# Performance work log

Measured on AMD Instinct MI355X. Metric: run time of the kernel, lower is better.

## Reference

```python
import jax, jax.numpy as jnp
import numpy as np
import math

D_MODEL = 1024
NUM_HEADS = 16
MAX_LEN = 2048
D_HEAD = D_MODEL // NUM_HEADS
BATCH = 2
SEQ = 2048


def setup_inputs() -> dict:
    root = jax.random.key(0)
    ks = jax.random.split(root, 10)
    s = 1.0 / math.sqrt(D_MODEL)
    return {
        "query": jax.random.normal(ks[0], (BATCH, SEQ, D_MODEL), jnp.float32),
        "key": jax.random.normal(ks[1], (BATCH, SEQ, D_MODEL), jnp.float32),
        "value": jax.random.normal(ks[2], (BATCH, SEQ, D_MODEL), jnp.float32),
        "Wq": jax.random.normal(ks[3], (D_MODEL, D_MODEL), jnp.float32) * s,
        "bq": jax.random.normal(ks[4], (D_MODEL,), jnp.float32) * s,
        "Wk": jax.random.normal(ks[5], (D_MODEL, D_MODEL), jnp.float32) * s,
        "bk": jax.random.normal(ks[6], (D_MODEL,), jnp.float32) * s,
        "Wv": jax.random.normal(ks[7], (D_MODEL, D_MODEL), jnp.float32) * s,
        "bv": jax.random.normal(ks[8], (D_MODEL,), jnp.float32) * s,
        "Er": jax.random.normal(ks[9], (MAX_LEN, D_HEAD), jnp.float32),
    }


def _skew(QEr):
    # QEr: [B, H, S, S] -> pad one zero column on the left, reshape, drop first row
    B, H, R, C = QEr.shape
    padded = jnp.pad(QEr, ((0, 0), (0, 0), (0, 0), (1, 0)))  # [B,H,R,C+1]
    reshaped = padded.reshape(B, H, C + 1, R)
    return reshaped[:, :, 1:, :]  # [B,H,R,C] == Srel


def reference(query, key, value, Wq, bq, Wk, bk, Wv, bv, Er):
    B, S, D = query.shape
    H, dh = NUM_HEADS, D_HEAD
    # nn.Linear: x @ W.T + b
    q = (jnp.einsum("bsd,ed->bse", query, Wq) + bq).reshape(B, S, H, dh).transpose(0, 2, 1, 3)  # [B,H,S,dh]
    k = (jnp.einsum("bsd,ed->bse", key, Wk) + bk).reshape(B, S, H, dh).transpose(0, 2, 1, 3)
    v = (jnp.einsum("bsd,ed->bse", value, Wv) + bv).reshape(B, S, H, dh).transpose(0, 2, 1, 3)
    start = MAX_LEN - S
    Er_s = Er[start:, :]  # [S, dh]
    QEr = jnp.einsum("bhsd,ld->bhsl", q, Er_s)  # [B,H,S,S]
    Srel = _skew(QEr)
    QK = jnp.einsum("bhsd,bhtd->bhst", q, k)
    attn = (QK + Srel) / math.sqrt(dh)
    causal = jnp.tril(jnp.ones((S, S), dtype=bool))
    attn = jnp.where(causal[None, None], attn, -jnp.inf)
    attn = jax.nn.softmax(attn, axis=-1)
    out = jnp.einsum("bhst,bhtd->bhsd", attn, v)  # [B,H,S,dh]
    out = out.transpose(0, 2, 1, 3).reshape(B, S, D)
    return out  # dropout is identity in eval mode
```

## Files before the change

kernel.cpp:

```cpp
#include <hip/hip_runtime.h>
#include <hip/hip_bf16.h>

typedef __attribute__((ext_vector_type(8))) short bf16x8;
typedef __attribute__((ext_vector_type(4))) float f32x4;

#define DEVI __device__ __forceinline__

constexpr int SEQ_   = 2048;
constexpr int HEADS  = 16;
constexpr int DHEAD  = 64;
constexpr int DMODEL = 1024;

DEVI unsigned short f2bf(float x) {
  __hip_bfloat16 h = __float2bfloat16(x);
  return __builtin_bit_cast(unsigned short, h);
}

DEVI f32x4 MFMA(bf16x8 a, bf16x8 b, f32x4 c) {
  return __builtin_amdgcn_mfma_f32_16x16x32_bf16(a, b, c, 0, 0, 0);
}

__global__ void conv3_kernel(const float* s0, const float* s1, const float* s2,
                             unsigned short* d0, unsigned short* d1, unsigned short* d2,
                             int n) {
  const float* s = (blockIdx.y == 0) ? s0 : (blockIdx.y == 1) ? s1 : s2;
  unsigned short* d = (blockIdx.y == 0) ? d0 : (blockIdx.y == 1) ? d1 : d2;
  int i = (blockIdx.x * 256 + threadIdx.x) * 8;
  if (i >= n) return;
  const float4* p = (const float4*)(s + i);
  float4 v0 = p[0], v1 = p[1];
  union { unsigned short u[8]; bf16x8 v; } t;
  t.u[0] = f2bf(v0.x); t.u[1] = f2bf(v0.y); t.u[2] = f2bf(v0.z); t.u[3] = f2bf(v0.w);
  t.u[4] = f2bf(v1.x); t.u[5] = f2bf(v1.y); t.u[6] = f2bf(v1.z); t.u[7] = f2bf(v1.w);
  *(bf16x8*)(d + i) = t.v;
}

__global__ __launch_bounds__(256) void proj3_kernel(
    const unsigned short* __restrict__ X0, const unsigned short* __restrict__ X1,
    const unsigned short* __restrict__ X2,
    const unsigned short* __restrict__ W0, const unsigned short* __restrict__ W1,
    const unsigned short* __restrict__ W2,
    const float* __restrict__ bi0, const float* __restrict__ bi1,
    const float* __restrict__ bi2,
    unsigned short* __restrict__ o0, unsigned short* __restrict__ o1,
    unsigned short* __restrict__ o2) {
  const int z = blockIdx.z;
  const unsigned short* X = (z == 0) ? X0 : (z == 1) ? X1 : X2;
  const unsigned short* W = (z == 0) ? W0 : (z == 1) ? W1 : W2;
  const float* bias        = (z == 0) ? bi0 : (z == 1) ? bi1 : bi2;
  unsigned short* out      = (z == 0) ? o0 : (z == 1) ? o1 : o2;

  __shared__ unsigned short Abuf[2][128 * 32];
  __shared__ unsigned short Bbuf[2][128 * 32];
  const int tid  = threadIdx.x;
  const int lane = tid & 63, wv = tid >> 6;
  const int q = lane >> 4, r = lane & 15;
  const int wrow = wv >> 1, wcol = wv & 1;
  const int rowA0 = blockIdx.x * 128, colB0 = blockIdx.y * 128;

  const char* Ag = (const char*)(X + (size_t)rowA0 * DMODEL);
  const char* Bg = (const char*)(W + (size_t)colB0 * DMODEL);

  f32x4 acc[4][4] = {};

  auto stage = [&](int ks, int buf) {
    const int koff = ks * 64;
#pragma unroll
    for (int i = 0; i < 2; ++i) {
      const int b   = (i * 256 + tid) * 16;
      const int row = b >> 6, col = b & 63;
      __builtin_amdgcn_global_load_lds(
          (const __attribute__((address_space(1))) void*)(Ag + (size_t)row * (DMODEL * 2) + koff + col),
          (__attribute__((address_space(3))) void*)((char*)&Abuf[buf][0] + i * 4096 + wv * 1024),
          16, 0, 0);
      __builtin_amdgcn_global_load_lds(
          (const __attribute__((address_space(1))) void*)(Bg + (size_t)row * (DMODEL * 2) + koff + col),
          (__attribute__((address_space(3))) void*)((char*)&Bbuf[buf][0] + i * 4096 + wv * 1024),
          16, 0, 0);
    }
  };

  stage(0, 0);
  for (int ks = 0; ks < 32; ++ks) {
    __syncthreads();
    if (ks + 1 < 32) stage(ks + 1, (ks + 1) & 1);
    const unsigned short* A  = &Abuf[ks & 1][0];
    const unsigned short* Bt = &Bbuf[ks & 1][0];
    bf16x8 af[4], bfr[4];
#pragma unroll
    for (int t = 0; t < 4; ++t) {
      af[t]  = *(const bf16x8*)(A  + (wrow * 64 + t * 16 + r) * 32 + q * 8);
      bfr[t] = *(const bf16x8*)(Bt + (wcol * 64 + t * 16 + r) * 32 + q * 8);
    }
#pragma unroll
    for (int m = 0; m < 4; ++m)
#pragma unroll
      for (int n = 0; n < 4; ++n)
        acc[m][n] = MFMA(af[m], bfr[n], acc[m][n]);
  }

#pragma unroll
  for (int m = 0; m < 4; ++m) {
#pragma unroll
    for (int n = 0; n < 4; ++n) {
      const int e  = colB0 + wcol * 64 + n * 16 + r;
      const float bv = bias[e];
      const int h = e >> 6, dd = e & 63;
      const int nrow0 = rowA0 + wrow * 64 + m * 16 + q * 4;
      const int bb = nrow0 >> 11, ss0 = nrow0 & 2047;
      const size_t bh = (size_t)(bb * HEADS + h);
      if (z == 0) {
#pragma unroll
        for (int j = 0; j < 4; ++j)
          out[(bh * SEQ_ + (ss0 + j)) * DHEAD + dd] = f2bf(acc[m][n][j] + bv);
      } else if (z == 1) {
#pragma unroll
        for (int j = 0; j < 4; ++j) {
          const int s = ss0 + j;
          const size_t off = (bh * 64 + (size_t)(s >> 5)) * 2048
                           + (size_t)(((dd >> 5) * 2 + ((s >> 4) & 1)) * 512)
                           + (size_t)(((((dd & 31) >> 3) << 4) + (s & 15)) * 8)
                           + (dd & 7);
          out[off] = f2bf(acc[m][n][j] + bv);
        }
      } else {
        union { unsigned short u[4]; uint2 v; } pk;
#pragma unroll
        for (int j = 0; j < 4; ++j) pk.u[j] = f2bf(acc[m][n][j] + bv);
        const size_t off = (bh * 64 + (size_t)(ss0 >> 5)) * 2048
                         + (size_t)((dd >> 4) * 512)
                         + (size_t)(((((ss0 & 31) >> 3) << 4) + (dd & 15)) * 8)
                         + (ss0 & 7);
        *(uint2*)&out[off] = pk.v;
      }
    }
  }
}

__global__ __launch_bounds__(128, 4) void attn_kernel(const unsigned short* __restrict__ qb,
                                                      const unsigned short* __restrict__ kt,
                                                      const unsigned short* __restrict__ vt,
                                                      const unsigned short* __restrict__ Er,
                                                      float* __restrict__ out,
                                                      float* __restrict__ pO,
                                                      float* __restrict__ pL) {
  __shared__ unsigned short k_lds[2][2048];
  __shared__ unsigned short v_lds[2][2048];
  __shared__ unsigned short p_lds[2][16][40];

  const int tid  = threadIdx.x;
  const int lane = tid & 63, wv = tid >> 6;
  const int q = lane >> 4, r = lane & 15;

  const int lid = blockIdx.x;
  const int xcd = lid & 7, idx = lid >> 3;
  const int bh  = (xcd << 2) | (idx & 3);
  const int rest = idx >> 2;
  const int p = rest >> 1, ab = rest & 1;
  const int Lt = 63 - p;
  const int sid = (bh << 5) | p;
  const int bb = bh >> 4, hh = bh & 15;

  const unsigned short* qbh = qb + (size_t)bh * SEQ_ * DHEAD;
  const char* ktb = (const char*)(kt + (size_t)bh * 64 * 2048);
  const char* vtb = (const char*)(vt + (size_t)bh * 64 * 2048);

  const f32x4 zero4 = {0.f, 0.f, 0.f, 0.f};

  auto stage = [&](int ktile, int buf) {
#pragma unroll
    for (int c = 0; c < 2; ++c) {
      __builtin_amdgcn_global_load_lds(
          (const __attribute__((address_space(1))) void*)(ktb + (size_t)ktile * 4096 + (c * 128 + tid) * 16),
          (__attribute__((address_space(3))) void*)((char*)&k_lds[buf][0] + c * 2048 + wv * 1024),
          16, 0, 0);
      __builtin_amdgcn_global_load_lds(
          (const __attribute__((address_space(1))) void*)(vtb + (size_t)ktile * 4096 + (c * 128 + tid) * 16),
          (__attribute__((address_space(3))) void*)((char*)&v_lds[buf][0] + c * 2048 + wv * 1024),
          16, 0, 0);
    }
  };

  auto run_strip = [&](int tile, int it0, int itN, float* po, float* pl) {
    const int s0 = tile * 32 + wv * 16;
    __syncthreads();
    stage(it0, 0);

    bf16x8 qf0 = *(const bf16x8*)(qbh + (size_t)(s0 + r) * DHEAD + q * 8);
    bf16x8 qf1 = *(const bf16x8*)(qbh + (size_t)(s0 + r) * DHEAD + 32 + q * 8);

    f32x4 oacc[4] = {};
    float lpart[4] = {0.f, 0.f, 0.f, 0.f};
    f32x4 qer0;
    {
      const int l0 = 2032 + it0 * 32 - s0 + r;
      bf16x8 e00 = *(const bf16x8*)(Er + (size_t)l0 * DHEAD + q * 8);
      bf16x8 e01 = *(const bf16x8*)(Er + (size_t)l0 * DHEAD + 32 + q * 8);
      qer0 = MFMA(qf1, e01, MFMA(qf0, e00, zero4));
    }

#pragma unroll 1
    for (int it = it0; it < itN; ++it) {
      const int cur = (it - it0) & 1;
      const int t0 = it * 32;
      const int lbase = 2032 + t0 - s0;

      __syncthreads();

      int l1 = lbase + 16 + r; l1 = l1 < 2047 ? l1 : 2047;
      int l2 = lbase + 32 + r; l2 = l2 < 2047 ? l2 : 2047;
      bf16x8 e10 = *(const bf16x8*)(Er + (size_t)l1 * DHEAD + q * 8);
      bf16x8 e11 = *(const bf16x8*)(Er + (size_t)l1 * DHEAD + 32 + q * 8);
      bf16x8 e20 = *(const bf16x8*)(Er + (size_t)l2 * DHEAD + q * 8);
      bf16x8 e21 = *(const bf16x8*)(Er + (size_t)l2 * DHEAD + 32 + q * 8);

      if (it + 1 < itN) stage(it + 1, 1 - cur);

      const unsigned short* KL = &k_lds[cur][0];
      const unsigned short* VL = &v_lds[cur][0];
      bf16x8 kf00 = *(const bf16x8*)(KL + lane * 8);
      bf16x8 kf10 = *(const bf16x8*)(KL + 512 + lane * 8);
      bf16x8 kf01 = *(const bf16x8*)(KL + 1024 + lane * 8);
      bf16x8 kf11 = *(const bf16x8*)(KL + 1536 + lane * 8);

      __builtin_amdgcn_s_setprio(1);
      f32x4 s40  = MFMA(qf1, kf01, MFMA(qf0, kf00, zero4));
      f32x4 s41  = MFMA(qf1, kf11, MFMA(qf0, kf10, zero4));
      f32x4 qer1 = MFMA(qf1, e11, MFMA(qf0, e10, zero4));
      f32x4 qer2 = MFMA(qf1, e21, MFMA(qf0, e20, zero4));
      __builtin_amdgcn_s_setprio(0);

#pragma unroll
      for (int j = 0; j < 4; ++j) {
        const int sl = q * 4 + j;
        const int idxw = r + 15 - sl;
        const int srcl = (q << 4) | (idxw & 15);
        const float g0 = __shfl(qer0[j], srcl);
        const float g1 = __shfl(qer1[j], srcl);
        const float g2 = __shfl(qer2[j], srcl);
        const bool lo = (idxw < 16);
        float sv0 = (s40[j] + (lo ? g0 : g1)) * 0.125f;
        float sv1 = (s41[j] + (lo ? g1 : g2)) * 0.125f;
        if (t0 + r      > s0 + sl) sv0 = -1e30f;
        if (t0 + 16 + r > s0 + sl) sv1 = -1e30f;
        const float p0 = __expf(sv0);
        const float p1 = __expf(sv1);
        lpart[j] += p0 + p1;
        p_lds[wv][sl][r]      = f2bf(p0);
        p_lds[wv][sl][16 + r] = f2bf(p1);
      }

      bf16x8 pf  = *(const bf16x8*)(&p_lds[wv][r][0] + q * 8);
      bf16x8 vf0 = *(const bf16x8*)(VL + lane * 8);
      bf16x8 vf1 = *(const bf16x8*)(VL + 512 + lane * 8);
      bf16x8 vf2 = *(const bf16x8*)(VL + 1024 + lane * 8);
      bf16x8 vf3 = *(const bf16x8*)(VL + 1536 + lane * 8);
      __builtin_amdgcn_s_setprio(1);
      oacc[0] = MFMA(pf, vf0, oacc[0]);
      oacc[1] = MFMA(pf, vf1, oacc[1]);
      oacc[2] = MFMA(pf, vf2, oacc[2]);
      oacc[3] = MFMA(pf, vf3, oacc[3]);
      __builtin_amdgcn_s_setprio(0);
      qer0 = qer2;
    }

#pragma unroll
    for (int j = 0; j < 4; ++j) {
      float ls = lpart[j];
#pragma unroll
      for (int d = 1; d < 16; d <<= 1) ls += __shfl_xor(ls, d);
      const int row = wv * 16 + q * 4 + j;
      if (po) {
#pragma unroll
        for (int dc = 0; dc < 4; ++dc)
          po[(size_t)row * 64 + dc * 16 + r] = oacc[dc][j];
        if (r == 0) pl[row] = ls;
      } else {
        const float inv = 1.0f / ls;
        const int ss = tile * 32 + row;
#pragma unroll
        for (int dc = 0; dc < 4; ++dc) {
          const int dd = dc * 16 + r;
          out[((size_t)(bb * SEQ_ + ss)) * DMODEL + hh * DHEAD + dd] = oacc[dc][j] * inv;
        }
      }
    }
  };

  if (ab == 0) {
    run_strip(Lt, 0, 32, pO + (size_t)(sid * 2) * 2048, pL + (size_t)(sid * 2) * 32);
  } else {
    run_strip(Lt, 32, 64 - p, pO + (size_t)(sid * 2 + 1) * 2048, pL + (size_t)(sid * 2 + 1) * 32);
    run_strip(p, 0, p + 1, nullptr, nullptr);
  }
}

__global__ __launch_bounds__(256) void reduce_kernel(const float* __restrict__ pO,
                                                     const float* __restrict__ pL,
                                                     float* __restrict__ out) {
  const int sid = blockIdx.x;
  const int bh = sid >> 5, p = sid & 31;
  const int bb = bh >> 4, hh = bh & 15;
  const int srow = (63 - p) * 32;
  const int tid = threadIdx.x;
  const int row = tid >> 3, dseg = (tid & 7) * 8;

  const float* a = pO + (size_t)(sid * 2) * 2048 + row * 64 + dseg;
  const float* b = a + 2048;
  const float la = pL[(size_t)(sid * 2) * 32 + row];
  const float lb = pL[(size_t)(sid * 2 + 1) * 32 + row];
  const float inv = 1.0f / (la + lb);

  float4 x0 = ((const float4*)a)[0], x1 = ((const float4*)a)[1];
  float4 y0 = ((const float4*)b)[0], y1 = ((const float4*)b)[1];
  float4 o0, o1;
  o0.x = (x0.x + y0.x) * inv; o0.y = (x0.y + y0.y) * inv;
  o0.z = (x0.z + y0.z) * inv; o0.w = (x0.w + y0.w) * inv;
  o1.x = (x1.x + y1.x) * inv; o1.y = (x1.y + y1.y) * inv;
  o1.z = (x1.z + y1.z) * inv; o1.w = (x1.w + y1.w) * inv;

  float* dst = out + ((size_t)(bb * SEQ_) + srow + row) * DMODEL + hh * DHEAD + dseg;
  ((float4*)dst)[0] = o0;
  ((float4*)dst)[1] = o1;
}

extern "C" void kernel_launch(void* const* d_in, const int* in_sizes, int n_in,
                              void* d_out, int out_size, void* d_ws, size_t ws_size,
                              hipStream_t stream) {
  const float* query = (const float*)d_in[0];
  const float* key   = (const float*)d_in[1];
  const float* value = (const float*)d_in[2];
  const float* Wq    = (const float*)d_in[3];
  const float* bq    = (const float*)d_in[4];
  const float* Wk    = (const float*)d_in[5];
  const float* bk    = (const float*)d_in[6];
  const float* Wv    = (const float*)d_in[7];
  const float* bv    = (const float*)d_in[8];
  const float* Er    = (const float*)d_in[9];

  char* ws = (char*)d_ws;
  unsigned short* qb   = (unsigned short*)(ws + (0u  << 20));
  unsigned short* ktil = (unsigned short*)(ws + (8u  << 20));
  unsigned short* vtil = (unsigned short*)(ws + (16u << 20));
  float*          pO   = (float*)(ws + (24u << 20));
  float*          pL   = (float*)(ws + (40u << 20));
  unsigned short* Xq   = (unsigned short*)(ws + (32u << 20));
  unsigned short* Xk   = (unsigned short*)(ws + (40u << 20));
  unsigned short* Xv   = (unsigned short*)(ws + (48u << 20));
  unsigned short* Wqb  = (unsigned short*)(ws + (56u << 20));
  unsigned short* Wkb  = (unsigned short*)(ws + (58u << 20));
  unsigned short* Wvb  = (unsigned short*)(ws + (60u << 20));
  unsigned short* Erb  = (unsigned short*)(ws + (62u << 20));

  conv3_kernel<<<dim3(2048, 3), 256, 0, stream>>>(query, key, value, Xq, Xk, Xv,
                                                  2 * SEQ_ * DMODEL);
  conv3_kernel<<<dim3(512, 3), 256, 0, stream>>>(Wq, Wk, Wv, Wqb, Wkb, Wvb,
                                                 DMODEL * DMODEL);
  conv3_kernel<<<dim3(64, 1), 256, 0, stream>>>(Er, Er, Er, Erb, Erb, Erb,
                                                SEQ_ * DHEAD);

  proj3_kernel<<<dim3(32, 8, 3), 256, 0, stream>>>(Xq, Xk, Xv, Wqb, Wkb, Wvb,
                                                   bq, bk, bv, qb, ktil, vtil);

  attn_kernel<<<dim3(2048), 128, 0, stream>>>(qb, ktil, vtil, Erb,
                                              (float*)d_out, pO, pL);

  reduce_kernel<<<dim3(1024), 256, 0, stream>>>(pO, pL, (float*)d_out);
}
```

Before: 155.3 us.

## Restructure relative attention into 128-row tiles with interleaved key-tile split

The attention kernel now runs 256-thread blocks, where each wave handles 32 query rows, so every staged K/V tile is shared across twice as many rows. Key tiles are split by parity between two blocks per query tile, and each block processes one long and one short tile to balance causal work. The reduce kernel is rewritten to combine those partials over 128-row tiles, and the 1/sqrt(dh) scale is folded into the Q projection epilogue. In exchange, each iteration does more Er loads and Er-projection MFMAs per row tile, since the old carried qer reuse is gone. The kernel also launches fewer blocks and needs more registers per thread.

New measurement: 155.9 us. Within noise of the previous version (+0.4%).

```diff
diff --git a/kernel.cpp b/kernel.cpp
--- a/kernel.cpp
+++ b/kernel.cpp
@@ -112,7 +112,7 @@
       if (z == 0) {
 #pragma unroll
         for (int j = 0; j < 4; ++j)
-          out[(bh * SEQ_ + (ss0 + j)) * DHEAD + dd] = f2bf(acc[m][n][j] + bv);
+          out[(bh * SEQ_ + (ss0 + j)) * DHEAD + dd] = f2bf((acc[m][n][j] + bv) * 0.125f);
       } else if (z == 1) {
 #pragma unroll
         for (int j = 0; j < 4; ++j) {
@@ -137,16 +137,13 @@
   }
 }
 
-__global__ __launch_bounds__(128, 4) void attn_kernel(const unsigned short* __restrict__ qb,
-                                                      const unsigned short* __restrict__ kt,
-                                                      const unsigned short* __restrict__ vt,
-                                                      const unsigned short* __restrict__ Er,
-                                                      float* __restrict__ out,
-                                                      float* __restrict__ pO,
-                                                      float* __restrict__ pL) {
+__global__ __launch_bounds__(256, 2) void attn_kernel(
+    const unsigned short* __restrict__ qb, const unsigned short* __restrict__ kt,
+    const unsigned short* __restrict__ vt, const unsigned short* __restrict__ Er,
+    float* __restrict__ pO, float* __restrict__ pL) {
   __shared__ unsigned short k_lds[2][2048];
   __shared__ unsigned short v_lds[2][2048];
-  __shared__ unsigned short p_lds[2][16][40];
+  __shared__ unsigned short p_lds[4][32][40];
 
   const int tid  = threadIdx.x;
   const int lane = tid & 63, wv = tid >> 6;
@@ -156,10 +153,7 @@
   const int xcd = lid & 7, idx = lid >> 3;
   const int bh  = (xcd << 2) | (idx & 3);
   const int rest = idx >> 2;
-  const int p = rest >> 1, ab = rest & 1;
-  const int Lt = 63 - p;
-  const int sid = (bh << 5) | p;
-  const int bb = bh >> 4, hh = bh & 15;
+  const int pairp = rest >> 1, ab = rest & 1;
 
   const unsigned short* qbh = qb + (size_t)bh * SEQ_ * DHEAD;
   const char* ktb = (const char*)(kt + (size_t)bh * 64 * 2048);
@@ -167,161 +161,169 @@
 
   const f32x4 zero4 = {0.f, 0.f, 0.f, 0.f};
 
-  auto stage = [&](int ktile, int buf) {
-#pragma unroll
-    for (int c = 0; c < 2; ++c) {
-      __builtin_amdgcn_global_load_lds(
-          (const __attribute__((address_space(1))) void*)(ktb + (size_t)ktile * 4096 + (c * 128 + tid) * 16),
-          (__attribute__((address_space(3))) void*)((char*)&k_lds[buf][0] + c * 2048 + wv * 1024),
-          16, 0, 0);
-      __builtin_amdgcn_global_load_lds(
-          (const __attribute__((address_space(1))) void*)(vtb + (size_t)ktile * 4096 + (c * 128 + tid) * 16),
-          (__attribute__((address_space(3))) void*)((char*)&v_lds[buf][0] + c * 2048 + wv * 1024),
-          16, 0, 0);
-    }
+  auto stage = [&](int kt2, int buf) {
+    __builtin_amdgcn_global_load_lds(
+        (const __attribute__((address_space(1))) void*)(ktb + (size_t)kt2 * 4096 + tid * 16),
+        (__attribute__((address_space(3))) void*)((char*)&k_lds[buf][0] + wv * 1024),
+        16, 0, 0);
+    __builtin_amdgcn_global_load_lds(
+        (const __attribute__((address_space(1))) void*)(vtb + (size_t)kt2 * 4096 + tid * 16),
+        (__attribute__((address_space(3))) void*)((char*)&v_lds[buf][0] + wv * 1024),
+        16, 0, 0);
   };
 
-  auto run_strip = [&](int tile, int it0, int itN, float* po, float* pl) {
-    const int s0 = tile * 32 + wv * 16;
+  auto run_strip = [&](int T, float* po, float* pl) {
+    const int s0 = T * 128 + wv * 32;
+    const int nK = 2 * T + 2;
     __syncthreads();
-    stage(it0, 0);
-
-    bf16x8 qf0 = *(const bf16x8*)(qbh + (size_t)(s0 + r) * DHEAD + q * 8);
-    bf16x8 qf1 = *(const bf16x8*)(qbh + (size_t)(s0 + r) * DHEAD + 32 + q * 8);
-
-    f32x4 oacc[4] = {};
-    float lpart[4] = {0.f, 0.f, 0.f, 0.f};
-    f32x4 qer0;
-    {
-      const int l0 = 2032 + it0 * 32 - s0 + r;
-      bf16x8 e00 = *(const bf16x8*)(Er + (size_t)l0 * DHEAD + q * 8);
-      bf16x8 e01 = *(const bf16x8*)(Er + (size_t)l0 * DHEAD + 32 + q * 8);
-      qer0 = MFMA(qf1, e01, MFMA(qf0, e00, zero4));
-    }
+    stage(ab, 0);
+
+    bf16x8 qf[2][2];
+#pragma unroll
+    for (int rt = 0; rt < 2; ++rt) {
+      qf[rt][0] = *(const bf16x8*)(qbh + (size_t)(s0 + rt * 16 + r) * DHEAD + q * 8);
+      qf[rt][1] = *(const bf16x8*)(qbh + (size_t)(s0 + rt * 16 + r) * DHEAD + 32 + q * 8);
+    }
+    f32x4 oacc[2][4] = {};
+    float lpart[2][4] = {};
 
 #pragma unroll 1
-    for (int it = it0; it < itN; ++it) {
-      const int cur = (it - it0) & 1;
-      const int t0 = it * 32;
-      const int lbase = 2032 + t0 - s0;
-
+    for (int k = 0; k < nK; ++k) {
+      const int buf = k & 1;
+      const int t0 = (2 * k + ab) * 32;
+      const bool active = (t0 <= s0 + 31);
       __syncthreads();
-
-      int l1 = lbase + 16 + r; l1 = l1 < 2047 ? l1 : 2047;
-      int l2 = lbase + 32 + r; l2 = l2 < 2047 ? l2 : 2047;
-      bf16x8 e10 = *(const bf16x8*)(Er + (size_t)l1 * DHEAD + q * 8);
-      bf16x8 e11 = *(const bf16x8*)(Er + (size_t)l1 * DHEAD + 32 + q * 8);
-      bf16x8 e20 = *(const bf16x8*)(Er + (size_t)l2 * DHEAD + q * 8);
-      bf16x8 e21 = *(const bf16x8*)(Er + (size_t)l2 * DHEAD + 32 + q * 8);
-
-      if (it + 1 < itN) stage(it + 1, 1 - cur);
-
-      const unsigned short* KL = &k_lds[cur][0];
-      const unsigned short* VL = &v_lds[cur][0];
+      if (k + 1 < nK) stage(2 * (k + 1) + ab, buf ^ 1);
+      if (!active) continue;
+
+      const int L0 = 2000 + t0 - s0;
+      bf16x8 ef[4][2];
+#pragma unroll
+      for (int m = 0; m < 4; ++m) {
+        int l = L0 + 16 * (m + 1) + r; l = l < 2047 ? l : 2047;
+        ef[m][0] = *(const bf16x8*)(Er + (size_t)l * DHEAD + q * 8);
+        ef[m][1] = *(const bf16x8*)(Er + (size_t)l * DHEAD + 32 + q * 8);
+      }
+
+      const unsigned short* KL = &k_lds[buf][0];
+      const unsigned short* VL = &v_lds[buf][0];
       bf16x8 kf00 = *(const bf16x8*)(KL + lane * 8);
       bf16x8 kf10 = *(const bf16x8*)(KL + 512 + lane * 8);
       bf16x8 kf01 = *(const bf16x8*)(KL + 1024 + lane * 8);
       bf16x8 kf11 = *(const bf16x8*)(KL + 1536 + lane * 8);
 
+      f32x4 s4[2][2], qer[2][4];
       __builtin_amdgcn_s_setprio(1);
-      f32x4 s40  = MFMA(qf1, kf01, MFMA(qf0, kf00, zero4));
-      f32x4 s41  = MFMA(qf1, kf11, MFMA(qf0, kf10, zero4));
-      f32x4 qer1 = MFMA(qf1, e11, MFMA(qf0, e10, zero4));
-      f32x4 qer2 = MFMA(qf1, e21, MFMA(qf0, e20, zero4));
+#pragma unroll
+      for (int rt = 0; rt < 2; ++rt) {
+        s4[rt][0] = MFMA(qf[rt][1], kf01, MFMA(qf[rt][0], kf00, zero4));
+        s4[rt][1] = MFMA(qf[rt][1], kf11, MFMA(qf[rt][0], kf10, zero4));
+      }
+#pragma unroll
+      for (int rt = 0; rt < 2; ++rt)
+#pragma unroll
+        for (int m = 0; m < 4; ++m)
+          qer[rt][m] = MFMA(qf[rt][1], ef[m][1], MFMA(qf[rt][0], ef[m][0], zero4));
       __builtin_amdgcn_s_setprio(0);
 
-#pragma unroll
-      for (int j = 0; j < 4; ++j) {
-        const int sl = q * 4 + j;
-        const int idxw = r + 15 - sl;
-        const int srcl = (q << 4) | (idxw & 15);
-        const float g0 = __shfl(qer0[j], srcl);
-        const float g1 = __shfl(qer1[j], srcl);
-        const float g2 = __shfl(qer2[j], srcl);
-        const bool lo = (idxw < 16);
-        float sv0 = (s40[j] + (lo ? g0 : g1)) * 0.125f;
-        float sv1 = (s41[j] + (lo ? g1 : g2)) * 0.125f;
-        if (t0 + r      > s0 + sl) sv0 = -1e30f;
-        if (t0 + 16 + r > s0 + sl) sv1 = -1e30f;
-        const float p0 = __expf(sv0);
-        const float p1 = __expf(sv1);
-        lpart[j] += p0 + p1;
-        p_lds[wv][sl][r]      = f2bf(p0);
-        p_lds[wv][sl][16 + r] = f2bf(p1);
-      }
-
-      bf16x8 pf  = *(const bf16x8*)(&p_lds[wv][r][0] + q * 8);
+      const int d0 = t0 - s0;
+#pragma unroll
+      for (int rt = 0; rt < 2; ++rt) {
+        const int base = rt ? 0 : 1;
+#pragma unroll
+        for (int j = 0; j < 4; ++j) {
+          const int sl = rt * 16 + q * 4 + j;
+          const int srcl = (q << 4) | ((47 + r - q * 4 - j) & 15);
+          const float sh0 = __shfl(qer[rt][base + 0][j], srcl);
+          const float sh1 = __shfl(qer[rt][base + 1][j], srcl);
+          const float sh2 = __shfl(qer[rt][base + 2][j], srcl);
+          const bool hi = (r > q * 4 + j);
+          const float g0 = hi ? sh1 : sh0;
+          const float g1 = hi ? sh2 : sh1;
+          const float sv0 = s4[rt][0][j] + g0;
+          const float sv1 = s4[rt][1][j] + g1;
+          const int a = sl - r;
+          const float p0 = (a >= d0)      ? __expf(sv0) : 0.f;
+          const float p1 = (a >= d0 + 16) ? __expf(sv1) : 0.f;
+          lpart[rt][j] += p0 + p1;
+          p_lds[wv][sl][r]      = f2bf(p0);
+          p_lds[wv][sl][16 + r] = f2bf(p1);
+        }
+      }
+
       bf16x8 vf0 = *(const bf16x8*)(VL + lane * 8);
       bf16x8 vf1 = *(const bf16x8*)(VL + 512 + lane * 8);
       bf16x8 vf2 = *(const bf16x8*)(VL + 1024 + lane * 8);
       bf16x8 vf3 = *(const bf16x8*)(VL + 1536 + lane * 8);
-      __builtin_amdgcn_s_setprio(1);
-      oacc[0] = MFMA(pf, vf0, oacc[0]);
-      oacc[1] = MFMA(pf, vf1, oacc[1]);
-      oacc[2] = MFMA(pf, vf2, oacc[2]);
-      oacc[3] = MFMA(pf, vf3, oacc[3]);
-      __builtin_amdgcn_s_setprio(0);
-      qer0 = qer2;
-    }
-
-#pragma unroll
-    for (int j = 0; j < 4; ++j) {
-      float ls = lpart[j];
-#pragma unroll
-      for (int d = 1; d < 16; d <<= 1) ls += __shfl_xor(ls, d);
-      const int row = wv * 16 + q * 4 + j;
-      if (po) {
+#pragma unroll
+      for (int rt = 0; rt < 2; ++rt) {
+        bf16x8 pf = *(const bf16x8*)(&p_lds[wv][rt * 16 + r][0] + q * 8);
+        __builtin_amdgcn_s_setprio(1);
+        oacc[rt][0] = MFMA(pf, vf0, oacc[rt][0]);
+        oacc[rt][1] = MFMA(pf, vf1, oacc[rt][1]);
+        oacc[rt][2] = MFMA(pf, vf2, oacc[rt][2]);
+        oacc[rt][3] = MFMA(pf, vf3, oacc[rt][3]);
+        __builtin_amdgcn_s_setprio(0);
+      }
+    }
+
+#pragma unroll
+    for (int rt = 0; rt < 2; ++rt)
+#pragma unroll
+      for (int j = 0; j < 4; ++j) {
+        float ls = lpart[rt][j];
+#pragma unroll
+        for (int d = 1; d < 16; d <<= 1) ls += __shfl_xor(ls, d);
+        const int row = wv * 32 + rt * 16 + q * 4 + j;
 #pragma unroll
         for (int dc = 0; dc < 4; ++dc)
-          po[(size_t)row * 64 + dc * 16 + r] = oacc[dc][j];
+          po[(size_t)row * 64 + dc * 16 + r] = oacc[rt][dc][j];
         if (r == 0) pl[row] = ls;
-      } else {
-        const float inv = 1.0f / ls;
-        const int ss = tile * 32 + row;
-#pragma unroll
-        for (int dc = 0; dc < 4; ++dc) {
-          const int dd = dc * 16 + r;
-          out[((size_t)(bb * SEQ_ + ss)) * DMODEL + hh * DHEAD + dd] = oacc[dc][j] * inv;
-        }
-      }
-    }
+      }
   };
 
-  if (ab == 0) {
-    run_strip(Lt, 0, 32, pO + (size_t)(sid * 2) * 2048, pL + (size_t)(sid * 2) * 32);
-  } else {
-    run_strip(Lt, 32, 64 - p, pO + (size_t)(sid * 2 + 1) * 2048, pL + (size_t)(sid * 2 + 1) * 32);
-    run_strip(p, 0, p + 1, nullptr, nullptr);
+  const int TL = 15 - pairp, TS = pairp;
+  {
+    const size_t slot = ((size_t)bh * 16 + TL) * 2 + ab;
+    run_strip(TL, pO + slot * 8192, pL + slot * 128);
+  }
+  {
+    const size_t slot = ((size_t)bh * 16 + TS) * 2 + ab;
+    run_strip(TS, pO + slot * 8192, pL + slot * 128);
   }
 }
 
 __global__ __launch_bounds__(256) void reduce_kernel(const float* __restrict__ pO,
                                                      const float* __restrict__ pL,
                                                      float* __restrict__ out) {
-  const int sid = blockIdx.x;
-  const int bh = sid >> 5, p = sid & 31;
+  const int slot = blockIdx.x;
+  const int bh = slot >> 4, tile = slot & 15;
   const int bb = bh >> 4, hh = bh & 15;
-  const int srow = (63 - p) * 32;
   const int tid = threadIdx.x;
-  const int row = tid >> 3, dseg = (tid & 7) * 8;
-
-  const float* a = pO + (size_t)(sid * 2) * 2048 + row * 64 + dseg;
-  const float* b = a + 2048;
-  const float la = pL[(size_t)(sid * 2) * 32 + row];
-  const float lb = pL[(size_t)(sid * 2 + 1) * 32 + row];
-  const float inv = 1.0f / (la + lb);
-
-  float4 x0 = ((const float4*)a)[0], x1 = ((const float4*)a)[1];
-  float4 y0 = ((const float4*)b)[0], y1 = ((const float4*)b)[1];
-  float4 o0, o1;
-  o0.x = (x0.x + y0.x) * inv; o0.y = (x0.y + y0.y) * inv;
-  o0.z = (x0.z + y0.z) * inv; o0.w = (x0.w + y0.w) * inv;
-  o1.x = (x1.x + y1.x) * inv; o1.y = (x1.y + y1.y) * inv;
-  o1.z = (x1.z + y1.z) * inv; o1.w = (x1.w + y1.w) * inv;
-
-  float* dst = out + ((size_t)(bb * SEQ_) + srow + row) * DMODEL + hh * DHEAD + dseg;
-  ((float4*)dst)[0] = o0;
-  ((float4*)dst)[1] = o1;
+  const int row0 = tid >> 3, c8 = (tid & 7) * 8;
+
+  const float* pA = pO + (size_t)slot * 16384;
+  const float* pB = pA + 8192;
+  const float* lA = pL + (size_t)slot * 256;
+  const float* lB = lA + 128;
+
+#pragma unroll
+  for (int rr = 0; rr < 4; ++rr) {
+    const int row = row0 + rr * 32;
+    const float inv = 1.0f / (lA[row] + lB[row]);
+    const float* a = pA + row * 64 + c8;
+    const float* b = pB + row * 64 + c8;
+    float4 x0 = ((const float4*)a)[0], x1 = ((const float4*)a)[1];
+    float4 y0 = ((const float4*)b)[0], y1 = ((const float4*)b)[1];
+    float4 o0, o1;
+    o0.x = (x0.x + y0.x) * inv; o0.y = (x0.y + y0.y) * inv;
+    o0.z = (x0.z + y0.z) * inv; o0.w = (x0.w + y0.w) * inv;
+    o1.x = (x1.x + y1.x) * inv; o1.y = (x1.y + y1.y) * inv;
+    o1.z = (x1.z + y1.z) * inv; o1.w = (x1.w + y1.w) * inv;
+    float* dst = out + ((size_t)(bb * SEQ_) + tile * 128 + row) * DMODEL + hh * DHEAD + c8;
+    ((float4*)dst)[0] = o0;
+    ((float4*)dst)[1] = o1;
+  }
 }
 
 extern "C" void kernel_launch(void* const* d_in, const int* in_sizes, int n_in,
@@ -343,7 +345,7 @@
   unsigned short* ktil = (unsigned short*)(ws + (8u  << 20));
   unsigned short* vtil = (unsigned short*)(ws + (16u << 20));
   float*          pO   = (float*)(ws + (24u << 20));
-  float*          pL   = (float*)(ws + (40u << 20));
+  float*          pL   = (float*)(ws + (60u << 20));
   unsigned short* Xq   = (unsigned short*)(ws + (32u << 20));
   unsigned short* Xk   = (unsigned short*)(ws + (40u << 20));
   unsigned short* Xv   = (unsigned short*)(ws + (48u << 20));
@@ -362,8 +364,7 @@
   proj3_kernel<<<dim3(32, 8, 3), 256, 0, stream>>>(Xq, Xk, Xv, Wqb, Wkb, Wvb,
                                                    bq, bk, bv, qb, ktil, vtil);
 
-  attn_kernel<<<dim3(2048), 128, 0, stream>>>(qb, ktil, vtil, Erb,
-                                              (float*)d_out, pO, pL);
-
-  reduce_kernel<<<dim3(1024), 256, 0, stream>>>(pO, pL, (float*)d_out);
-}
+  attn_kernel<<<dim3(512), 256, 0, stream>>>(qb, ktil, vtil, Erb, pO, pL);
+
+  reduce_kernel<<<dim3(512), 256, 0, stream>>>(pO, pL, (float*)d_out);
+}
```
